# Kernel optimization log

Hardware: AMD Instinct MI355X
Metric: run time of the kernel (lower is better)

Reference implementation:

```python
import jax, jax.numpy as jnp
from jax import lax
import numpy as np

N_CLUSTERS = 8
G_CLUSTERS = 2
D_DIM = 512
DN = ('NCHW', 'OIHW', 'NCHW')


def _conv(x, w, b):
    y = lax.conv_general_dilated(x, w, window_strides=(1, 1), padding='VALID',
                                 dimension_numbers=DN)
    return y + b[None, :, None, None]


def setup_inputs() -> dict:
    key = jax.random.key(0)
    ks = jax.random.split(key, 6)
    B, D, H, W = 32, D_DIM, 7, 250
    KG = N_CLUSTERS + G_CLUSTERS
    scale = 1.0 / np.sqrt(D * 7)
    return {
        'x': jax.random.normal(ks[0], (B, D, H, W), dtype=jnp.float32),
        'feat_w': jax.random.normal(ks[1], (D, D, 7, 1), dtype=jnp.float32) * scale,
        'feat_b': jax.random.normal(ks[2], (D,), dtype=jnp.float32) * 0.01,
        'assign_w': jax.random.normal(ks[3], (KG, D, 7, 1), dtype=jnp.float32) * scale,
        'assign_b': jax.random.normal(ks[4], (KG,), dtype=jnp.float32) * 0.01,
        'centroids': jax.random.uniform(ks[5], (D, KG), dtype=jnp.float32),
    }


def reference(x, feat_w, feat_b, assign_w, assign_b, centroids):
    # features branch: conv(7,1) + ReLU -> (B, D, H', W)
    feat = jnp.maximum(_conv(x, feat_w, feat_b), 0.0)
    # assignment branch: conv(7,1) -> softmax over clusters -> (B, K+G, H', W)
    soft = jax.nn.softmax(_conv(x, assign_w, assign_b), axis=1)
    # Fused VLAD aggregation (mathematically identical to
    # sum_hw soft[b,k,hw] * (feat[b,d,hw] - centroids[d,k]) without
    # materializing the (B,D,K+G,H',W) residual tensor):
    s_sum = soft.sum(axis=(-2, -1))                                # (B, K+G)
    agg = jnp.einsum('bkhw,bdhw->bdk', soft, feat)                 # (B, D, K+G)
    cluster_res = agg - centroids[None, :, :] * s_sum[:, None, :]  # (B, D, K+G)
    cluster_res = cluster_res[..., :N_CLUSTERS]                    # drop ghost clusters
    # L2 normalize over feature dim (torch F.normalize, eps=1e-12)
    norm = jnp.sqrt(jnp.sum(cluster_res * cluster_res, axis=1, keepdims=True))
    cluster_l2 = cluster_res / jnp.maximum(norm, 1e-12)
    # (B, D, K) -> (B, K, D) -> (B, K*D)
    out = jnp.swapaxes(cluster_l2, 1, 2).reshape(x.shape[0], N_CLUSTERS * D_DIM)
    return out
```

## Files before the change

### kernel.cpp

```cpp
#include <hip/hip_runtime.h>
#include <stdint.h>

typedef float f32x4 __attribute__((ext_vector_type(4)));
typedef __bf16 bf16x8 __attribute__((ext_vector_type(8)));
typedef unsigned short ushortx8 __attribute__((ext_vector_type(8)));

#define D_DIM 512
#define KGC 10
#define NCLU 8
#define BATCH 32
#define WPOS 250
#define WPAD 256
#define KDIM 3584
#define MROWS 522
#define MPAD 528
#define WROWS 640

__device__ __forceinline__ float bf2f(unsigned short u) {
  union { unsigned int i; float f; } v; v.i = ((unsigned int)u) << 16; return v.f;
}
__device__ __forceinline__ unsigned short f2bf(float f) {
  union { float f; unsigned int i; } v; v.f = f;
  unsigned int r = v.i + 0x7FFFu + ((v.i >> 16) & 1u);
  return (unsigned short)(r >> 16);
}

__device__ __forceinline__ void load_lds16(const void* g, void* l) {
  __builtin_amdgcn_global_load_lds(
      (const __attribute__((address_space(1))) void*)g,
      (__attribute__((address_space(3))) void*)l, 16, 0, 0);
}

__global__ void prep_kernel(const float* __restrict__ fw,
                            const float* __restrict__ fb,
                            const float* __restrict__ aw,
                            const float* __restrict__ ab,
                            unsigned short* __restrict__ Wcat,
                            float* __restrict__ bcat) {
  int r = blockIdx.x;
  unsigned short* dst = Wcat + (size_t)r * KDIM;
  const float* src = (r < D_DIM) ? (fw + (size_t)r * KDIM)
                   : (r < MROWS) ? (aw + (size_t)(r - D_DIM) * KDIM)
                                 : nullptr;
  for (int i = threadIdx.x; i < KDIM / 4; i += 256) {
    unsigned short o0 = 0, o1 = 0, o2 = 0, o3 = 0;
    if (src) {
      float4 v = ((const float4*)src)[i];
      o0 = f2bf(v.x); o1 = f2bf(v.y); o2 = f2bf(v.z); o3 = f2bf(v.w);
    }
    ushortx8 dummy;
    ushort4 o; o.x = o0; o.y = o1; o.z = o2; o.w = o3;
    ((ushort4*)dst)[i] = o;
  }
  if (threadIdx.x == 0)
    bcat[r] = r < D_DIM ? fb[r] : (r < MROWS ? ab[r - D_DIM] : 0.f);
}

__global__ __launch_bounds__(256) void transpose_kernel(
    const float* __restrict__ x, unsigned short* __restrict__ Xt) {
  __shared__ unsigned short tile[64][66];
  const int kt = blockIdx.x * 64, nt = blockIdx.y * 64, b = blockIdx.z;
  const float* xb = x + (size_t)b * (KDIM * WPOS);
  const int t = threadIdx.x;
#pragma unroll
  for (int it = 0; it < 8; it++) {
    int id = it * 256 + t;
    int k = id >> 5, p = id & 31;
    int n = nt + p * 2;
    float vx = 0.f, vy = 0.f;
    if (n < WPOS) {
      float2 v = *(const float2*)&xb[(size_t)(kt + k) * WPOS + n];
      vx = v.x; vy = v.y;
    }
    ushort2 o; o.x = f2bf(vx); o.y = f2bf(vy);
    *(ushort2*)&tile[k][p * 2] = o;
  }
  __syncthreads();
  unsigned short* xtb = Xt + (size_t)(b * WPAD + nt) * KDIM;
#pragma unroll
  for (int it = 0; it < 8; it++) {
    int id = it * 256 + t;
    int n = id >> 5, q = id & 31;
    ushort2 o; o.x = tile[2 * q][n]; o.y = tile[2 * q + 1][n];
    *(ushort2*)&xtb[(size_t)n * KDIM + kt + 2 * q] = o;
  }
}

#define BM 128
#define BN 64
#define BK 64

__global__ __launch_bounds__(256) void gemm_kernel(
    const unsigned short* __restrict__ Xt, const unsigned short* __restrict__ Wcat,
    const float* __restrict__ bcat, unsigned short* __restrict__ Y) {
  __shared__ __align__(16) unsigned short Wl[BM * BK];
  __shared__ __align__(16) unsigned short Xl[BN * BK];
  const int tid = threadIdx.x;
  const int mt = blockIdx.x, ntg = blockIdx.y;
  const int lane = tid & 63, wv = tid >> 6;
  const unsigned short* Wg = Wcat + (size_t)mt * BM * KDIM;
  const unsigned short* Xg = Xt + (size_t)ntg * BN * KDIM;

  const f32x4 zero = {0.f, 0.f, 0.f, 0.f};
  f32x4 acc[2][4];
#pragma unroll
  for (int i = 0; i < 2; i++)
#pragma unroll
    for (int j = 0; j < 4; j++) acc[i][j] = zero;

  const int wm = wv * 32;
  const int fr = lane & 15, kg = lane >> 4;
  const int sx = fr & 7;

  for (int kb = 0; kb < KDIM; kb += BK) {
    __syncthreads();
#pragma unroll
    for (int i = 0; i < 4; i++) {
      int s = i * 256 + tid;
      int row = s >> 3, p = s & 7;
      int blk = p ^ (row & 7);
      load_lds16(Wg + (size_t)row * KDIM + kb + blk * 8, &Wl[s * 8]);
    }
#pragma unroll
    for (int i = 0; i < 2; i++) {
      int s = i * 256 + tid;
      int row = s >> 3, p = s & 7;
      int blk = p ^ (row & 7);
      load_lds16(Xg + (size_t)row * KDIM + kb + blk * 8, &Xl[s * 8]);
    }
    __syncthreads();
#pragma unroll
    for (int ks = 0; ks < BK; ks += 32) {
      const int kb8 = (ks >> 3) + kg;
      bf16x8 af[2], bfr[4];
#pragma unroll
      for (int i = 0; i < 2; i++)
        af[i] = *(const bf16x8*)&Wl[(wm + i * 16 + fr) * BK + (kb8 ^ sx) * 8];
#pragma unroll
      for (int j = 0; j < 4; j++)
        bfr[j] = *(const bf16x8*)&Xl[(j * 16 + fr) * BK + (kb8 ^ sx) * 8];
#pragma unroll
      for (int i = 0; i < 2; i++)
#pragma unroll
        for (int j = 0; j < 4; j++)
          acc[i][j] = __builtin_amdgcn_mfma_f32_16x16x32_bf16(af[i], bfr[j], acc[i][j], 0, 0, 0);
    }
  }

  const int b = ntg >> 2;
  const int nb = (ntg & 3) * BN;
  unsigned short* Yb = Y + (size_t)b * MPAD * WPAD;
  const int m0 = mt * BM + wm + kg * 4;
  const int n0 = nb + fr;
#pragma unroll
  for (int i = 0; i < 2; i++) {
#pragma unroll
    for (int r = 0; r < 4; r++) {
      int m = m0 + i * 16 + r;
      if (m < MPAD) {
        float bias = bcat[m];
#pragma unroll
        for (int j = 0; j < 4; j++) {
          float v = acc[i][j][r] + bias;
          if (m < D_DIM) v = fmaxf(v, 0.f);
          Yb[(size_t)m * WPAD + n0 + j * 16] = f2bf(v);
        }
      }
    }
  }
}

__global__ __launch_bounds__(256) void epi_kernel(
    const unsigned short* __restrict__ Y, const float* __restrict__ cent,
    float* __restrict__ out) {
  __shared__ float soft[WPAD];
  __shared__ float red[4];
  const int b = blockIdx.x >> 3, k = blockIdx.x & 7;
  const int tid = threadIdx.x;
  const unsigned short* Yb = Y + (size_t)b * MPAD * WPAD;

  float sv = 0.f;
  if (tid < WPOS) {
    float lg[KGC];
    float mx = -1e30f;
#pragma unroll
    for (int j = 0; j < KGC; j++) {
      lg[j] = bf2f(Yb[(size_t)(D_DIM + j) * WPAD + tid]);
      mx = fmaxf(mx, lg[j]);
    }
    float s = 0.f, ek = 0.f;
#pragma unroll
    for (int j = 0; j < KGC; j++) {
      float e = __expf(lg[j] - mx);
      s += e;
      if (j == k) ek = e;
    }
    sv = ek / s;
  }
  soft[tid] = sv;
  __syncthreads();

  float v = sv;
#pragma unroll
  for (int o = 32; o > 0; o >>= 1) v += __shfl_down(v, o, 64);
  if ((tid & 63) == 0) red[tid >> 6] = v;
  __syncthreads();
  float ssum = red[0] + red[1] + red[2] + red[3];

  float a0 = 0.f, a1 = 0.f;
  const unsigned short* row0 = Yb + (size_t)tid * WPAD;
  const unsigned short* row1 = Yb + (size_t)(tid + 256) * WPAD;
  for (int w = 0; w < WPAD; w += 8) {
    ushortx8 f0 = *(const ushortx8*)(row0 + w);
    ushortx8 f1 = *(const ushortx8*)(row1 + w);
#pragma unroll
    for (int u = 0; u < 8; u++) {
      float s = soft[w + u];
      a0 += bf2f(f0[u]) * s;
      a1 += bf2f(f1[u]) * s;
    }
  }
  float c0 = a0 - cent[(size_t)tid * KGC + k] * ssum;
  float c1 = a1 - cent[(size_t)(tid + 256) * KGC + k] * ssum;

  __syncthreads();
  float q = c0 * c0 + c1 * c1;
#pragma unroll
  for (int o = 32; o > 0; o >>= 1) q += __shfl_down(q, o, 64);
  if ((tid & 63) == 0) red[tid >> 6] = q;
  __syncthreads();
  float norm = sqrtf(red[0] + red[1] + red[2] + red[3]);
  float inv = 1.f / fmaxf(norm, 1e-12f);

  float* ob = out + (size_t)b * (NCLU * D_DIM) + (size_t)k * D_DIM;
  ob[tid] = c0 * inv;
  ob[tid + 256] = c1 * inv;
}

extern "C" void kernel_launch(void* const* d_in, const int* in_sizes, int n_in,
                              void* d_out, int out_size, void* d_ws, size_t ws_size,
                              hipStream_t stream) {
  const float* x  = (const float*)d_in[0];
  const float* fw = (const float*)d_in[1];
  const float* fb = (const float*)d_in[2];
  const float* aw = (const float*)d_in[3];
  const float* ab = (const float*)d_in[4];
  const float* ce = (const float*)d_in[5];
  float* out = (float*)d_out;
  char* ws = (char*)d_ws;

  const size_t XT_BYTES = (size_t)BATCH * WPAD * KDIM * 2;
  const size_t WC_BYTES = (size_t)WROWS * KDIM * 2;
  const size_t BC_BYTES = (size_t)WROWS * 4;
  unsigned short* Xt = (unsigned short*)(ws);
  unsigned short* Wc = (unsigned short*)(ws + XT_BYTES);
  float*          bc = (float*)(ws + XT_BYTES + WC_BYTES);
  unsigned short* Yv = (unsigned short*)(ws + XT_BYTES + WC_BYTES + BC_BYTES);

  prep_kernel<<<WROWS, 256, 0, stream>>>(fw, fb, aw, ab, Wc, bc);
  transpose_kernel<<<dim3(KDIM / 64, WPAD / 64, BATCH), 256, 0, stream>>>(x, Xt);
  gemm_kernel<<<dim3(5, 128), 256, 0, stream>>>(Xt, Wc, bc, Yv);
  epi_kernel<<<BATCH * NCLU, 256, 0, stream>>>(Yv, ce, out);
}
```

Baseline: 261.7 us.

## Split assignment GEMM into split-K kernel and widen transpose accesses

The fused GEMM used to compute a fifth 128-row tile that held only 10 useful assignment rows. That tile is dropped from the feature GEMM, which now launches 4 M-tiles. A separate small kernel computes the 16 assignment rows, with each of its four waves handling one quarter of K and the partial sums reduced through LDS. The transpose kernel now reads 4 floats and writes 8 bf16 values per thread to cut instruction count. The cost of this is an extra kernel launch, plus strided LDS column reads in the transpose.

```diff
diff --git a/kernel.cpp b/kernel.cpp
--- a/kernel.cpp
+++ b/kernel.cpp
@@ -48,7 +48,6 @@
       float4 v = ((const float4*)src)[i];
       o0 = f2bf(v.x); o1 = f2bf(v.y); o2 = f2bf(v.z); o3 = f2bf(v.w);
     }
-    ushortx8 dummy;
     ushort4 o; o.x = o0; o.y = o1; o.z = o2; o.w = o3;
     ((ushort4*)dst)[i] = o;
   }
@@ -63,26 +62,33 @@
   const float* xb = x + (size_t)b * (KDIM * WPOS);
   const int t = threadIdx.x;
 #pragma unroll
-  for (int it = 0; it < 8; it++) {
+  for (int it = 0; it < 4; it++) {
     int id = it * 256 + t;
-    int k = id >> 5, p = id & 31;
-    int n = nt + p * 2;
-    float vx = 0.f, vy = 0.f;
+    int k = id >> 4, p = id & 15;
+    int n = nt + p * 4;
+    const float* row = xb + (size_t)(kt + k) * WPOS;
+    float v0 = 0.f, v1 = 0.f, v2 = 0.f, v3 = 0.f;
     if (n < WPOS) {
-      float2 v = *(const float2*)&xb[(size_t)(kt + k) * WPOS + n];
-      vx = v.x; vy = v.y;
-    }
-    ushort2 o; o.x = f2bf(vx); o.y = f2bf(vy);
-    *(ushort2*)&tile[k][p * 2] = o;
+      float2 a = *(const float2*)&row[n];
+      v0 = a.x; v1 = a.y;
+    }
+    if (n + 3 < WPOS) {
+      float2 bq = *(const float2*)&row[n + 2];
+      v2 = bq.x; v3 = bq.y;
+    }
+    ushort4 o; o.x = f2bf(v0); o.y = f2bf(v1); o.z = f2bf(v2); o.w = f2bf(v3);
+    *(ushort4*)&tile[k][p * 4] = o;
   }
   __syncthreads();
   unsigned short* xtb = Xt + (size_t)(b * WPAD + nt) * KDIM;
 #pragma unroll
-  for (int it = 0; it < 8; it++) {
+  for (int it = 0; it < 2; it++) {
     int id = it * 256 + t;
-    int n = id >> 5, q = id & 31;
-    ushort2 o; o.x = tile[2 * q][n]; o.y = tile[2 * q + 1][n];
-    *(ushort2*)&xtb[(size_t)n * KDIM + kt + 2 * q] = o;
+    int n = id >> 3, q = id & 7;
+    ushortx8 o;
+#pragma unroll
+    for (int r = 0; r < 8; r++) o[r] = tile[8 * q + r][n];
+    *(ushortx8*)&xtb[(size_t)n * KDIM + kt + 8 * q] = o;
   }
 }
 
@@ -90,7 +96,7 @@
 #define BN 64
 #define BK 64
 
-__global__ __launch_bounds__(256) void gemm_kernel(
+__global__ __launch_bounds__(256) void gemm_feat(
     const unsigned short* __restrict__ Xt, const unsigned short* __restrict__ Wcat,
     const float* __restrict__ bcat, unsigned short* __restrict__ Y) {
   __shared__ __align__(16) unsigned short Wl[BM * BK];
@@ -157,16 +163,80 @@
 #pragma unroll
     for (int r = 0; r < 4; r++) {
       int m = m0 + i * 16 + r;
-      if (m < MPAD) {
-        float bias = bcat[m];
-#pragma unroll
-        for (int j = 0; j < 4; j++) {
-          float v = acc[i][j][r] + bias;
-          if (m < D_DIM) v = fmaxf(v, 0.f);
-          Yb[(size_t)m * WPAD + n0 + j * 16] = f2bf(v);
-        }
+      float bias = bcat[m];
+#pragma unroll
+      for (int j = 0; j < 4; j++) {
+        float v = fmaxf(acc[i][j][r] + bias, 0.f);
+        Yb[(size_t)m * WPAD + n0 + j * 16] = f2bf(v);
       }
     }
+  }
+}
+
+__global__ __launch_bounds__(256) void gemm_assign(
+    const unsigned short* __restrict__ Xt, const unsigned short* __restrict__ Wcat,
+    const float* __restrict__ bcat, unsigned short* __restrict__ Y) {
+  __shared__ __align__(16) unsigned short Wl[4 * 16 * 64];
+  __shared__ __align__(16) unsigned short Xl[4 * 32 * 64];
+  __shared__ float Pl[4][16][32];
+  const int tid = threadIdx.x;
+  const int blk_n = blockIdx.x;
+  const int n0 = blk_n * 32;
+  const int lane = tid & 63, wv = tid >> 6;
+  const int fr = lane & 15, kg = lane >> 4;
+  const int sx = fr & 7;
+
+  const f32x4 zero = {0.f, 0.f, 0.f, 0.f};
+  f32x4 acc[2];
+  acc[0] = zero; acc[1] = zero;
+
+  for (int i = 0; i < 14; i++) {
+    __syncthreads();
+#pragma unroll
+    for (int it = 0; it < 2; it++) {
+      int s = it * 256 + tid;
+      int wd = s >> 7, r = (s >> 3) & 15, p = s & 7;
+      int blk = p ^ (r & 7);
+      load_lds16(Wcat + (size_t)(D_DIM + r) * KDIM + wd * 896 + i * 64 + blk * 8,
+                 &Wl[s * 8]);
+    }
+#pragma unroll
+    for (int it = 0; it < 4; it++) {
+      int s = it * 256 + tid;
+      int wd = s >> 8, r = (s >> 3) & 31, p = s & 7;
+      int blk = p ^ (r & 7);
+      load_lds16(Xt + (size_t)(n0 + r) * KDIM + wd * 896 + i * 64 + blk * 8,
+                 &Xl[s * 8]);
+    }
+    __syncthreads();
+#pragma unroll
+    for (int ks = 0; ks < 64; ks += 32) {
+      const int kb8 = (ks >> 3) + kg;
+      bf16x8 af = *(const bf16x8*)&Wl[(wv * 16 + fr) * 64 + (kb8 ^ sx) * 8];
+#pragma unroll
+      for (int j = 0; j < 2; j++) {
+        bf16x8 bfr = *(const bf16x8*)&Xl[(wv * 32 + j * 16 + fr) * 64 + (kb8 ^ sx) * 8];
+        acc[j] = __builtin_amdgcn_mfma_f32_16x16x32_bf16(af, bfr, acc[j], 0, 0, 0);
+      }
+    }
+  }
+
+  __syncthreads();
+#pragma unroll
+  for (int j = 0; j < 2; j++)
+#pragma unroll
+    for (int r = 0; r < 4; r++)
+      Pl[wv][kg * 4 + r][j * 16 + fr] = acc[j][r];
+  __syncthreads();
+
+#pragma unroll
+  for (int it = 0; it < 2; it++) {
+    int o = it * 256 + tid;
+    int m = o >> 5, n = o & 31;
+    float v = Pl[0][m][n] + Pl[1][m][n] + Pl[2][m][n] + Pl[3][m][n] + bcat[D_DIM + m];
+    int ng = n0 + n;
+    int b = ng >> 8, col = ng & 255;
+    Y[(size_t)b * MPAD * WPAD + (size_t)(D_DIM + m) * WPAD + col] = f2bf(v);
   }
 }
 
@@ -257,8 +327,9 @@
   float*          bc = (float*)(ws + XT_BYTES + WC_BYTES);
   unsigned short* Yv = (unsigned short*)(ws + XT_BYTES + WC_BYTES + BC_BYTES);
 
-  prep_kernel<<<WROWS, 256, 0, stream>>>(fw, fb, aw, ab, Wc, bc);
+  prep_kernel<<<MPAD, 256, 0, stream>>>(fw, fb, aw, ab, Wc, bc);
   transpose_kernel<<<dim3(KDIM / 64, WPAD / 64, BATCH), 256, 0, stream>>>(x, Xt);
-  gemm_kernel<<<dim3(5, 128), 256, 0, stream>>>(Xt, Wc, bc, Yv);
+  gemm_feat<<<dim3(4, 128), 256, 0, stream>>>(Xt, Wc, bc, Yv);
+  gemm_assign<<<256, 256, 0, stream>>>(Xt, Wc, bc, Yv);
   epi_kernel<<<BATCH * NCLU, 256, 0, stream>>>(Yv, ce, out);
 }
```

Measured after the change: 266.5 us. About the same (+1.8%).

## Fuse x transpose/convert into GEMM, split-K with full-M tiles and reduce kernel

Applied to the files above, without the earlier changes.

Drops the separate transpose kernel. The GEMM now reads fp32 x directly, converts it to bf16 in registers and writes it to LDS, prefetching the next K step. Each block covers all 544 weight rows for one 64-column tile, with K split four ways to keep enough blocks in flight. Partial sums are written in fp32 and combined by a new reduce kernel that applies bias and ReLU. This removes the bf16 Xt round trip through memory and the reloading of X across M tiles, at the cost of a large fp32 partial buffer, a large LDS footprint and high register pressure.

```diff
diff --git a/kernel.cpp b/kernel.cpp
--- a/kernel.cpp
+++ b/kernel.cpp
@@ -14,7 +14,11 @@
 #define KDIM 3584
 #define MROWS 522
 #define MPAD 528
-#define WROWS 640
+#define MBIG 544
+#define KSPLIT 4
+#define KCHUNK 896
+#define NSTEPS 14
+#define NTILES 128
 
 __device__ __forceinline__ float bf2f(unsigned short u) {
   union { unsigned int i; float f; } v; v.i = ((unsigned int)u) << 16; return v.f;
@@ -48,7 +52,6 @@
       float4 v = ((const float4*)src)[i];
       o0 = f2bf(v.x); o1 = f2bf(v.y); o2 = f2bf(v.z); o3 = f2bf(v.w);
     }
-    ushortx8 dummy;
     ushort4 o; o.x = o0; o.y = o1; o.z = o2; o.w = o3;
     ((ushort4*)dst)[i] = o;
   }
@@ -56,118 +59,143 @@
     bcat[r] = r < D_DIM ? fb[r] : (r < MROWS ? ab[r - D_DIM] : 0.f);
 }
 
-__global__ __launch_bounds__(256) void transpose_kernel(
-    const float* __restrict__ x, unsigned short* __restrict__ Xt) {
-  __shared__ unsigned short tile[64][66];
-  const int kt = blockIdx.x * 64, nt = blockIdx.y * 64, b = blockIdx.z;
-  const float* xb = x + (size_t)b * (KDIM * WPOS);
-  const int t = threadIdx.x;
-#pragma unroll
-  for (int it = 0; it < 8; it++) {
-    int id = it * 256 + t;
-    int k = id >> 5, p = id & 31;
-    int n = nt + p * 2;
-    float vx = 0.f, vy = 0.f;
-    if (n < WPOS) {
-      float2 v = *(const float2*)&xb[(size_t)(kt + k) * WPOS + n];
-      vx = v.x; vy = v.y;
-    }
-    ushort2 o; o.x = f2bf(vx); o.y = f2bf(vy);
-    *(ushort2*)&tile[k][p * 2] = o;
-  }
-  __syncthreads();
-  unsigned short* xtb = Xt + (size_t)(b * WPAD + nt) * KDIM;
-#pragma unroll
-  for (int it = 0; it < 8; it++) {
-    int id = it * 256 + t;
-    int n = id >> 5, q = id & 31;
-    ushort2 o; o.x = tile[2 * q][n]; o.y = tile[2 * q + 1][n];
-    *(ushort2*)&xtb[(size_t)n * KDIM + kt + 2 * q] = o;
-  }
-}
-
-#define BM 128
-#define BN 64
-#define BK 64
-
-__global__ __launch_bounds__(256) void gemm_kernel(
-    const unsigned short* __restrict__ Xt, const unsigned short* __restrict__ Wcat,
-    const float* __restrict__ bcat, unsigned short* __restrict__ Y) {
-  __shared__ __align__(16) unsigned short Wl[BM * BK];
-  __shared__ __align__(16) unsigned short Xl[BN * BK];
+__global__ __launch_bounds__(256, 2) void gemm_fused(
+    const float* __restrict__ x, const unsigned short* __restrict__ Wcat,
+    float* __restrict__ P) {
+  __shared__ __align__(16) unsigned short Wl[MBIG * 64];
+  __shared__ __align__(16) unsigned short Xl[64 * 64];
   const int tid = threadIdx.x;
-  const int mt = blockIdx.x, ntg = blockIdx.y;
+  const int nt = blockIdx.x, sp = blockIdx.y;
+  const int b = nt >> 2, n0 = (nt & 3) * 64;
   const int lane = tid & 63, wv = tid >> 6;
-  const unsigned short* Wg = Wcat + (size_t)mt * BM * KDIM;
-  const unsigned short* Xg = Xt + (size_t)ntg * BN * KDIM;
-
-  const f32x4 zero = {0.f, 0.f, 0.f, 0.f};
-  f32x4 acc[2][4];
-#pragma unroll
-  for (int i = 0; i < 2; i++)
-#pragma unroll
-    for (int j = 0; j < 4; j++) acc[i][j] = zero;
-
-  const int wm = wv * 32;
   const int fr = lane & 15, kg = lane >> 4;
   const int sx = fr & 7;
-
-  for (int kb = 0; kb < KDIM; kb += BK) {
+  const int nloc = tid & 63;
+  const int nglob = n0 + nloc;
+  const bool okn = nglob < WPOS;
+  const int kb0 = tid >> 6;
+  const float* xb = x + (size_t)b * KDIM * WPOS + nglob;
+  const int kbase = sp * KCHUNK;
+
+  float vx[16];
+#pragma unroll
+  for (int pass = 0; pass < 2; pass++) {
+    int kb = kb0 + 4 * pass;
+#pragma unroll
+    for (int e = 0; e < 8; e++) {
+      int k = kbase + kb * 8 + e;
+      vx[pass * 8 + e] = okn ? xb[(size_t)k * WPOS] : 0.f;
+    }
+  }
+
+  const f32x4 zero = {0.f, 0.f, 0.f, 0.f};
+  f32x4 acc[8][4];
+#pragma unroll
+  for (int i = 0; i < 8; i++)
+#pragma unroll
+    for (int j = 0; j < 4; j++) acc[i][j] = zero;
+  f32x4 acca = zero;
+
+  for (int st = 0; st < NSTEPS; st++) {
+    const int kst = kbase + st * 64;
     __syncthreads();
 #pragma unroll
-    for (int i = 0; i < 4; i++) {
-      int s = i * 256 + tid;
+    for (int pass = 0; pass < 2; pass++) {
+      int kb = kb0 + 4 * pass;
+      ushortx8 pk;
+#pragma unroll
+      for (int e = 0; e < 8; e++) pk[e] = f2bf(vx[pass * 8 + e]);
+      *(ushortx8*)&Xl[nloc * 64 + (kb ^ (nloc & 7)) * 8] = pk;
+    }
+#pragma unroll
+    for (int it = 0; it < 17; it++) {
+      int s = it * 256 + tid;
       int row = s >> 3, p = s & 7;
       int blk = p ^ (row & 7);
-      load_lds16(Wg + (size_t)row * KDIM + kb + blk * 8, &Wl[s * 8]);
-    }
-#pragma unroll
-    for (int i = 0; i < 2; i++) {
-      int s = i * 256 + tid;
-      int row = s >> 3, p = s & 7;
-      int blk = p ^ (row & 7);
-      load_lds16(Xg + (size_t)row * KDIM + kb + blk * 8, &Xl[s * 8]);
+      load_lds16(Wcat + (size_t)row * KDIM + kst + blk * 8, &Wl[s * 8]);
     }
     __syncthreads();
-#pragma unroll
-    for (int ks = 0; ks < BK; ks += 32) {
-      const int kb8 = (ks >> 3) + kg;
-      bf16x8 af[2], bfr[4];
-#pragma unroll
-      for (int i = 0; i < 2; i++)
-        af[i] = *(const bf16x8*)&Wl[(wm + i * 16 + fr) * BK + (kb8 ^ sx) * 8];
-#pragma unroll
-      for (int j = 0; j < 4; j++)
-        bfr[j] = *(const bf16x8*)&Xl[(j * 16 + fr) * BK + (kb8 ^ sx) * 8];
-#pragma unroll
-      for (int i = 0; i < 2; i++)
-#pragma unroll
-        for (int j = 0; j < 4; j++)
-          acc[i][j] = __builtin_amdgcn_mfma_f32_16x16x32_bf16(af[i], bfr[j], acc[i][j], 0, 0, 0);
-    }
-  }
-
-  const int b = ntg >> 2;
-  const int nb = (ntg & 3) * BN;
-  unsigned short* Yb = Y + (size_t)b * MPAD * WPAD;
-  const int m0 = mt * BM + wm + kg * 4;
-  const int n0 = nb + fr;
-#pragma unroll
-  for (int i = 0; i < 2; i++) {
-#pragma unroll
-    for (int r = 0; r < 4; r++) {
-      int m = m0 + i * 16 + r;
-      if (m < MPAD) {
-        float bias = bcat[m];
-#pragma unroll
-        for (int j = 0; j < 4; j++) {
-          float v = acc[i][j][r] + bias;
-          if (m < D_DIM) v = fmaxf(v, 0.f);
-          Yb[(size_t)m * WPAD + n0 + j * 16] = f2bf(v);
+    if (st + 1 < NSTEPS) {
+      const int kst2 = kst + 64;
+#pragma unroll
+      for (int pass = 0; pass < 2; pass++) {
+        int kb = kb0 + 4 * pass;
+#pragma unroll
+        for (int e = 0; e < 8; e++) {
+          int k = kst2 + kb * 8 + e;
+          vx[pass * 8 + e] = okn ? xb[(size_t)k * WPOS] : 0.f;
         }
       }
     }
-  }
+#pragma unroll
+    for (int ks = 0; ks < 64; ks += 32) {
+      const int off = (((ks >> 3) + kg) ^ sx) * 8;
+      bf16x8 bfr[4];
+#pragma unroll
+      for (int j = 0; j < 4; j++)
+        bfr[j] = *(const bf16x8*)&Xl[(j * 16 + fr) * 64 + off];
+      {
+        bf16x8 aas = *(const bf16x8*)&Wl[(512 + fr) * 64 + off];
+        bf16x8 bfa = *(const bf16x8*)&Xl[(wv * 16 + fr) * 64 + off];
+        acca = __builtin_amdgcn_mfma_f32_16x16x32_bf16(aas, bfa, acca, 0, 0, 0);
+      }
+#pragma unroll
+      for (int i = 0; i < 8; i++) {
+        bf16x8 af = *(const bf16x8*)&Wl[(wv * 128 + i * 16 + fr) * 64 + off];
+#pragma unroll
+        for (int j = 0; j < 4; j++)
+          acc[i][j] = __builtin_amdgcn_mfma_f32_16x16x32_bf16(af, bfr[j], acc[i][j], 0, 0, 0);
+      }
+    }
+  }
+
+  float* Pb = P + (size_t)(sp * NTILES + nt) * (MBIG * 64);
+#pragma unroll
+  for (int i = 0; i < 8; i++) {
+#pragma unroll
+    for (int r = 0; r < 4; r++) {
+      int m = wv * 128 + i * 16 + kg * 4 + r;
+#pragma unroll
+      for (int j = 0; j < 4; j++)
+        Pb[(size_t)m * 64 + j * 16 + fr] = acc[i][j][r];
+    }
+  }
+#pragma unroll
+  for (int r = 0; r < 4; r++)
+    Pb[(size_t)(512 + kg * 4 + r) * 64 + wv * 16 + fr] = acca[r];
+}
+
+__global__ __launch_bounds__(256) void reduce_kernel(
+    const float* __restrict__ P, const float* __restrict__ bcat,
+    unsigned short* __restrict__ Y) {
+  const int nt = blockIdx.x, mg = blockIdx.y;
+  const int t = threadIdx.x;
+  const int m = mg * 32 + (t >> 3);
+  const int nl = (t & 7) * 8;
+  if (m >= MPAD) return;
+  const size_t base = (size_t)nt * (MBIG * 64) + (size_t)m * 64 + nl;
+  const size_t spstr = (size_t)NTILES * (MBIG * 64);
+  float s[8];
+#pragma unroll
+  for (int e = 0; e < 8; e++) s[e] = 0.f;
+#pragma unroll
+  for (int sp = 0; sp < KSPLIT; sp++) {
+    const float* p = P + sp * spstr + base;
+    float4 a = *(const float4*)p;
+    float4 c = *(const float4*)(p + 4);
+    s[0] += a.x; s[1] += a.y; s[2] += a.z; s[3] += a.w;
+    s[4] += c.x; s[5] += c.y; s[6] += c.z; s[7] += c.w;
+  }
+  float bias = bcat[m];
+  ushortx8 o;
+#pragma unroll
+  for (int e = 0; e < 8; e++) {
+    float v = s[e] + bias;
+    if (m < D_DIM) v = fmaxf(v, 0.f);
+    o[e] = f2bf(v);
+  }
+  const int bb = nt >> 2, c0 = (nt & 3) * 64 + nl;
+  *(ushortx8*)&Y[(size_t)bb * MPAD * WPAD + (size_t)m * WPAD + c0] = o;
 }
 
 __global__ __launch_bounds__(256) void epi_kernel(
@@ -249,16 +277,16 @@
   float* out = (float*)d_out;
   char* ws = (char*)d_ws;
 
-  const size_t XT_BYTES = (size_t)BATCH * WPAD * KDIM * 2;
-  const size_t WC_BYTES = (size_t)WROWS * KDIM * 2;
-  const size_t BC_BYTES = (size_t)WROWS * 4;
-  unsigned short* Xt = (unsigned short*)(ws);
-  unsigned short* Wc = (unsigned short*)(ws + XT_BYTES);
-  float*          bc = (float*)(ws + XT_BYTES + WC_BYTES);
-  unsigned short* Yv = (unsigned short*)(ws + XT_BYTES + WC_BYTES + BC_BYTES);
-
-  prep_kernel<<<WROWS, 256, 0, stream>>>(fw, fb, aw, ab, Wc, bc);
-  transpose_kernel<<<dim3(KDIM / 64, WPAD / 64, BATCH), 256, 0, stream>>>(x, Xt);
-  gemm_kernel<<<dim3(5, 128), 256, 0, stream>>>(Xt, Wc, bc, Yv);
+  const size_t WC_BYTES = (size_t)640 * KDIM * 2;
+  const size_t BC_BYTES = 4096;
+  const size_t P_BYTES  = (size_t)KSPLIT * NTILES * MBIG * 64 * 4;
+  unsigned short* Wc = (unsigned short*)(ws);
+  float*          bc = (float*)(ws + WC_BYTES);
+  float*          P  = (float*)(ws + WC_BYTES + BC_BYTES);
+  unsigned short* Yv = (unsigned short*)(ws + WC_BYTES + BC_BYTES + P_BYTES);
+
+  prep_kernel<<<MBIG, 256, 0, stream>>>(fw, fb, aw, ab, Wc, bc);
+  gemm_fused<<<dim3(NTILES, KSPLIT), 256, 0, stream>>>(x, Wc, P);
+  reduce_kernel<<<dim3(NTILES, 17), 256, 0, stream>>>(P, bc, Yv);
   epi_kernel<<<BATCH * NCLU, 256, 0, stream>>>(Yv, ce, out);
 }
```

Result: faster. 255.6 us (-2.3%).
